# Performance work log

Hardware: AMD Instinct MI355X
Metric: run time of the kernel (lower is better)

## Reference

```python
import jax, jax.numpy as jnp
import numpy as np
import math

B, N, M = 4, 2048, 2048
DIM_Q = DIM_K = DIM_V = 1024
H = 16

def setup_inputs() -> dict:
    key = jax.random.key(0)
    ks = jax.random.split(key, 10)
    s = 0.02
    return {
        "Q": jax.random.normal(ks[0], (B, N, DIM_Q), jnp.float32),
        "K": jax.random.normal(ks[1], (B, M, DIM_K), jnp.float32),
        "Wq": jax.random.normal(ks[2], (DIM_V, DIM_Q), jnp.float32) * s,
        "bq": jax.random.normal(ks[3], (DIM_V,), jnp.float32) * s,
        "Wk": jax.random.normal(ks[4], (DIM_V, DIM_K), jnp.float32) * s,
        "bk": jax.random.normal(ks[5], (DIM_V,), jnp.float32) * s,
        "Wv": jax.random.normal(ks[6], (DIM_V, DIM_K), jnp.float32) * s,
        "bv": jax.random.normal(ks[7], (DIM_V,), jnp.float32) * s,
        "Wo": jax.random.normal(ks[8], (DIM_V, DIM_V), jnp.float32) * s,
        "bo": jax.random.normal(ks[9], (DIM_V,), jnp.float32) * s,
    }

def reference(Q, K, Wq, bq, Wk, bk, Wv, bv, Wo, bo):
    d = DIM_V // H  # head dim
    Qp = Q @ Wq.T + bq            # [B,N,DIM_V]
    Kp = K @ Wk.T + bk            # [B,M,DIM_V]
    Vp = K @ Wv.T + bv            # [B,M,DIM_V]
    # split heads: [B,T,H,d] -> [B,H,T,d]
    Qh = Qp.reshape(B, N, H, d).transpose(0, 2, 1, 3)
    Kh = Kp.reshape(B, M, H, d).transpose(0, 2, 1, 3)
    Vh = Vp.reshape(B, M, H, d).transpose(0, 2, 1, 3)
    # NOTE: original scales by sqrt(dim_V), not sqrt(head_dim)
    scores = jnp.einsum('bhnd,bhmd->bhnm', Qh, Kh) / math.sqrt(DIM_V)
    A = jax.nn.softmax(scores, axis=-1)
    Oh = Qh + jnp.einsum('bhnm,bhmd->bhnd', A, Vh)   # residual with projected Q
    O = Oh.transpose(0, 2, 1, 3).reshape(B, N, DIM_V)
    O = O + jax.nn.relu(O @ Wo.T + bo)
    return O
```

## Files before the change

kernel.cpp:

```cpp
#include <hip/hip_runtime.h>
#include <cstddef>
#include <cstdint>


typedef unsigned short ushort_t;
typedef __attribute__((ext_vector_type(8))) short bf16x8;
typedef __attribute__((ext_vector_type(4))) float floatx4;
typedef __attribute__((ext_vector_type(2))) float f32x2;
typedef __attribute__((ext_vector_type(2))) __bf16 b16x2;
typedef __attribute__((ext_vector_type(4))) unsigned short us4;

__device__ __forceinline__ ushort_t f2bf(float x) {
  union { float f; unsigned u; } v; v.f = x;
  unsigned r = v.u + 0x7FFFu + ((v.u >> 16) & 1u);
  return (ushort_t)(r >> 16);
}
__device__ __forceinline__ float bf2f(ushort_t x) {
  union { unsigned u; float f; } v; v.u = ((unsigned)x) << 16;
  return v.f;
}
__device__ __forceinline__ unsigned pk2(float a, float b) {
  union { float f; unsigned u; } x, y; x.f = a; y.f = b;
  return __builtin_amdgcn_perm(y.u + 0x8000u, x.u + 0x8000u, 0x07060302u);
}
__device__ __forceinline__ unsigned pk2c(float a, float b) {
  union { b16x2 v; unsigned u; } r;
  r.v = __builtin_convertvector((f32x2){a, b}, b16x2);
  return r.u;
}
__device__ __forceinline__ floatx4 mfma16(bf16x8 a, bf16x8 b, floatx4 c) {
  return __builtin_amdgcn_mfma_f32_16x16x32_bf16(a, b, c, 0, 0, 0);
}
__device__ __forceinline__ void gld_lds16(const void* g, void* l) {
  __builtin_amdgcn_global_load_lds(
      (const __attribute__((address_space(1))) unsigned int*)g,
      (__attribute__((address_space(3))) unsigned int*)l, 16, 0, 0);
}

__global__ void cvt6(const float* __restrict__ i0, const float* __restrict__ i1,
                     const float* __restrict__ i2, const float* __restrict__ i3,
                     const float* __restrict__ i4, const float* __restrict__ i5,
                     ushort_t* __restrict__ o0, ushort_t* __restrict__ o1,
                     ushort_t* __restrict__ o2, ushort_t* __restrict__ o3,
                     ushort_t* __restrict__ o4, ushort_t* __restrict__ o5) {
  int z = blockIdx.z;
  const float* in = z == 0 ? i0 : z == 1 ? i1 : z == 2 ? i2 : z == 3 ? i3 : z == 4 ? i4 : i5;
  ushort_t* out = z == 0 ? o0 : z == 1 ? o1 : z == 2 ? o2 : z == 3 ? o3 : z == 4 ? o4 : o5;
  int n8 = (z < 2) ? 1048576 : 131072;
  int i = blockIdx.x * 256 + threadIdx.x;
  if (i < n8) {
    const float4* p = (const float4*)in + (size_t)i * 2;
    float4 a = p[0], b = p[1];
    uint4 o;
    o.x = pk2(a.x, a.y); o.y = pk2(a.z, a.w);
    o.z = pk2(b.x, b.y); o.w = pk2(b.z, b.w);
    *((uint4*)out + i) = o;
  }
}

__global__ __launch_bounds__(256, 2)
void gemm_qkv(const ushort_t* __restrict__ Qb, const ushort_t* __restrict__ Kb,
              const ushort_t* __restrict__ Wqb, const ushort_t* __restrict__ Wkb,
              const ushort_t* __restrict__ Wvb,
              const float* __restrict__ bq, const float* __restrict__ bk,
              const float* __restrict__ bv,
              ushort_t* __restrict__ Qp, ushort_t* __restrict__ Kp,
              ushort_t* __restrict__ Vt)
{
  const int Kd = 1024, Nn = 1024;
  const int z = blockIdx.z;
  const ushort_t* Ab = (z == 0) ? Qb : Kb;
  const ushort_t* Bw = (z == 0) ? Wqb : (z == 1) ? Wkb : Wvb;
  const float* bias  = (z == 0) ? bq : (z == 1) ? bk : bv;

  __shared__ __align__(16) ushort_t As[128][64];
  __shared__ __align__(16) ushort_t Bs[128][64];
  const int tid = threadIdx.x;
  const int lane = tid & 63, wave = tid >> 6;
  const int wm = (wave >> 1) * 64, wn = (wave & 1) * 64;
  const int rq = lane & 15, kg = lane >> 4;

  const int wg = blockIdx.x, xcd = wg & 7, slot = wg >> 3;
  const int by = xcd * 8 + (slot >> 3);
  const int bx = slot & 7;
  const int row0 = by * 128, col0 = bx * 128;

  const int st_sub = lane >> 3;
  const int st_cs  = (lane & 7) ^ st_sub;

  floatx4 acc[4][4];
#pragma unroll
  for (int i = 0; i < 4; ++i)
#pragma unroll
    for (int j = 0; j < 4; ++j) acc[i][j] = (floatx4){0.f, 0.f, 0.f, 0.f};

  for (int k0 = 0; k0 < Kd; k0 += 64) {
    __syncthreads();
#pragma unroll
    for (int r = 0; r < 4; ++r) {
      int i = wave * 4 + r;
      int row = i * 8 + st_sub;
      gld_lds16(Ab + (size_t)(row0 + row) * Kd + k0 + st_cs * 8, (ushort_t*)As + i * 512);
      gld_lds16(Bw + (size_t)(col0 + row) * Kd + k0 + st_cs * 8, (ushort_t*)Bs + i * 512);
    }
    __syncthreads();
#pragma unroll
    for (int kq = 0; kq < 2; ++kq) {
      bf16x8 af[4], bfr[4];
#pragma unroll
      for (int mi = 0; mi < 4; ++mi)
        af[mi] = *(const bf16x8*)&As[wm + mi*16 + rq][((kq*4 + kg) ^ (rq & 7)) * 8];
#pragma unroll
      for (int ni = 0; ni < 4; ++ni)
        bfr[ni] = *(const bf16x8*)&Bs[wn + ni*16 + rq][((kq*4 + kg) ^ (rq & 7)) * 8];
#pragma unroll
      for (int mi = 0; mi < 4; ++mi)
#pragma unroll
        for (int ni = 0; ni < 4; ++ni)
          acc[mi][ni] = mfma16(af[mi], bfr[ni], acc[mi][ni]);
    }
  }

  float bv4[4];
#pragma unroll
  for (int ni = 0; ni < 4; ++ni) bv4[ni] = bias[col0 + wn + ni*16 + rq];

  if (z < 2) {
    ushort_t* Cb = (z == 0) ? Qp : Kp;
#pragma unroll
    for (int mi = 0; mi < 4; ++mi)
#pragma unroll
      for (int ni = 0; ni < 4; ++ni)
#pragma unroll
        for (int rr = 0; rr < 4; ++rr) {
          int row = row0 + wm + mi*16 + kg*4 + rr;
          int col = col0 + wn + ni*16 + rq;
          Cb[(size_t)row * Nn + col] = f2bf(acc[mi][ni][rr] + bv4[ni]);
        }
  } else {
#pragma unroll
    for (int mi = 0; mi < 4; ++mi)
#pragma unroll
      for (int ni = 0; ni < 4; ++ni) {
        int col = col0 + wn + ni*16 + rq;
        int h = col >> 6, dvb = (col >> 4) & 3;
        int kvg = row0 + wm + (mi >> 1) * 32;
        int bI = kvg >> 11, kv = kvg & 2047;
        int t = kv >> 7, c = (kv >> 5) & 3;
        size_t addr = (size_t)(bI * 16 + h) * 131072 + t * 8192
                    + (c * 4 + dvb) * 512 + (kg * 16 + rq) * 8 + (mi & 1) * 4;
        us4 o = { f2bf(acc[mi][ni][0] + bv4[ni]), f2bf(acc[mi][ni][1] + bv4[ni]),
                  f2bf(acc[mi][ni][2] + bv4[ni]), f2bf(acc[mi][ni][3] + bv4[ni]) };
        *(us4*)(Vt + addr) = o;
      }
  }
}

__global__ __launch_bounds__(256, 2)
void gemm_out(const ushort_t* __restrict__ Ob, const ushort_t* __restrict__ Bw,
              const float* __restrict__ bias, float* __restrict__ Out)
{
  const int Kd = 1024, Nn = 1024;
  __shared__ __align__(16) ushort_t As[128][64];
  __shared__ __align__(16) ushort_t Bs[128][64];
  const int tid = threadIdx.x;
  const int lane = tid & 63, wave = tid >> 6;
  const int wm = (wave >> 1) * 64, wn = (wave & 1) * 64;
  const int rq = lane & 15, kg = lane >> 4;

  const int wg = blockIdx.x, xcd = wg & 7, slot = wg >> 3;
  const int by = xcd * 8 + (slot >> 3);
  const int bx = slot & 7;
  const int row0 = by * 128, col0 = bx * 128;

  const int st_sub = lane >> 3;
  const int st_cs  = (lane & 7) ^ st_sub;

  floatx4 acc[4][4];
#pragma unroll
  for (int i = 0; i < 4; ++i)
#pragma unroll
    for (int j = 0; j < 4; ++j) acc[i][j] = (floatx4){0.f, 0.f, 0.f, 0.f};

  for (int k0 = 0; k0 < Kd; k0 += 64) {
    __syncthreads();
#pragma unroll
    for (int r = 0; r < 4; ++r) {
      int i = wave * 4 + r;
      int row = i * 8 + st_sub;
      gld_lds16(Ob + (size_t)(row0 + row) * Kd + k0 + st_cs * 8, (ushort_t*)As + i * 512);
      gld_lds16(Bw + (size_t)(col0 + row) * Kd + k0 + st_cs * 8, (ushort_t*)Bs + i * 512);
    }
    __syncthreads();
#pragma unroll
    for (int kq = 0; kq < 2; ++kq) {
      bf16x8 af[4], bfr[4];
#pragma unroll
      for (int mi = 0; mi < 4; ++mi)
        af[mi] = *(const bf16x8*)&As[wm + mi*16 + rq][((kq*4 + kg) ^ (rq & 7)) * 8];
#pragma unroll
      for (int ni = 0; ni < 4; ++ni)
        bfr[ni] = *(const bf16x8*)&Bs[wn + ni*16 + rq][((kq*4 + kg) ^ (rq & 7)) * 8];
#pragma unroll
      for (int mi = 0; mi < 4; ++mi)
#pragma unroll
        for (int ni = 0; ni < 4; ++ni)
          acc[mi][ni] = mfma16(af[mi], bfr[ni], acc[mi][ni]);
    }
  }

  float bv4[4];
#pragma unroll
  for (int ni = 0; ni < 4; ++ni) bv4[ni] = bias[col0 + wn + ni*16 + rq];
#pragma unroll
  for (int mi = 0; mi < 4; ++mi)
#pragma unroll
    for (int ni = 0; ni < 4; ++ni)
#pragma unroll
      for (int rr = 0; rr < 4; ++rr) {
        int row = row0 + wm + mi*16 + kg*4 + rr;
        int col = col0 + wn + ni*16 + rq;
        size_t idx = (size_t)row * Nn + col;
        float pre = acc[mi][ni][rr] + bv4[ni];
        Out[idx] = bf2f(Ob[idx]) + (pre > 0.f ? pre : 0.f);
      }
}

__global__ __launch_bounds__(256, 2)
void attn_kernel(const ushort_t* __restrict__ Qp,
                 const ushort_t* __restrict__ Kp,
                 const ushort_t* __restrict__ Vt,
                 ushort_t* __restrict__ Ob)
{
  const float sc2 = 0.045084439f;
  const int wg = blockIdx.x, xcd = wg & 7, slot = wg >> 3;
  const int bh = xcd * 8 + (slot >> 4);
  const int qt = slot & 15;
  const int b = bh >> 4, h = bh & 15;
  const int q0 = qt * 128;

  __shared__ __align__(16) ushort_t Ks[2][8192];

  const int tid = threadIdx.x, lane = tid & 63, wq = tid >> 6;
  const int rq = lane & 15, kg = lane >> 4;

  const size_t qkbase = (size_t)(b * 2048) * 1024 + h * 64;
  const ushort_t* vbase = Vt + (size_t)bh * 131072 + lane * 8;

  const int sg_sub = lane >> 3;
  const int sg_csk = (lane & 7) ^ sg_sub;

#pragma unroll
  for (int r = 0; r < 4; ++r) {
    int i = wq * 4 + r;
    int row = i * 8 + sg_sub;
    gld_lds16(Qp + qkbase + (size_t)(q0 + row) * 1024 + sg_csk * 8, &Ks[1][i * 512]);
  }
  __syncthreads();

  auto stage = [&](int kt, int bufi) {
    const int kv0 = kt * 128;
#pragma unroll
    for (int r = 0; r < 4; ++r) {
      int i = wq * 4 + r;
      int rowk = i * 8 + sg_sub;
      gld_lds16(Kp + qkbase + (size_t)(kv0 + rowk) * 1024 + sg_csk * 8,
                &Ks[bufi][i * 512]);
    }
  };
  stage(0, 0);

  bf16x8 aq[2][2];
#pragma unroll
  for (int ni = 0; ni < 2; ++ni)
#pragma unroll
    for (int kq = 0; kq < 2; ++kq) {
      int row = wq * 32 + ni * 16 + rq;
      int ch = (kq * 4 + kg) ^ (rq & 7);
      bf16x8 t = *(const bf16x8*)&Ks[1][row * 64 + ch * 8];
#pragma unroll
      for (int e = 0; e < 8; ++e)
        t[e] = (short)f2bf(bf2f((ushort_t)t[e]) * sc2);
      aq[ni][kq] = t;
    }

  bf16x8 ones;
#pragma unroll
  for (int e = 0; e < 8; ++e) ones[e] = (short)0x3F80;

  const floatx4 zf = (floatx4){0.f, 0.f, 0.f, 0.f};

  floatx4 oacc[2][4];
  floatx4 lacc[2];
#pragma unroll
  for (int nb = 0; nb < 2; ++nb) {
    lacc[nb] = (floatx4){0.f,0.f,0.f,0.f};
#pragma unroll
    for (int dvb = 0; dvb < 4; ++dvb) oacc[nb][dvb] = (floatx4){0.f,0.f,0.f,0.f};
  }

  __syncthreads();

  int cur = 0;
#pragma unroll 2
  for (int kt = 0; kt < 16; ++kt) {
    const ushort_t* vtile = vbase + kt * 8192;

    bf16x8 vfa[16];
#pragma unroll
    for (int j = 0; j < 16; ++j)
      vfa[j] = *(const bf16x8*)(vtile + j * 512);

    if (kt < 15) stage(kt + 1, cur ^ 1);

    floatx4 s[8][2];
    __builtin_amdgcn_s_setprio(1);
    {
      bf16x8 ak[8];
#pragma unroll
      for (int mi = 0; mi < 8; ++mi)
        ak[mi] = *(const bf16x8*)&Ks[cur][(mi * 16 + rq) * 64 + ((kg ^ (rq & 7)) * 8)];
#pragma unroll
      for (int mi = 0; mi < 8; ++mi)
#pragma unroll
        for (int ni = 0; ni < 2; ++ni)
          s[mi][ni] = mfma16(ak[mi], aq[ni][0], zf);
#pragma unroll
      for (int mi = 0; mi < 8; ++mi)
        ak[mi] = *(const bf16x8*)&Ks[cur][(mi * 16 + rq) * 64 + (((4 + kg) ^ (rq & 7)) * 8)];
#pragma unroll
      for (int mi = 0; mi < 8; ++mi)
#pragma unroll
        for (int ni = 0; ni < 2; ++ni)
          s[mi][ni] = mfma16(ak[mi], aq[ni][1], s[mi][ni]);
    }
    __builtin_amdgcn_s_setprio(0);

#pragma unroll
    for (int mi = 0; mi < 2; ++mi)
#pragma unroll
      for (int ni = 0; ni < 2; ++ni)
#pragma unroll
        for (int rr = 0; rr < 4; ++rr)
          s[mi][ni][rr] = __builtin_amdgcn_exp2f(s[mi][ni][rr]);

#pragma unroll
    for (int c = 0; c < 4; ++c) {
      union { unsigned u[4]; bf16x8 v; } pa0, pa1;
      pa0.u[0] = pk2c(s[2*c  ][0][0], s[2*c  ][0][1]);
      pa0.u[1] = pk2c(s[2*c  ][0][2], s[2*c  ][0][3]);
      pa0.u[2] = pk2c(s[2*c+1][0][0], s[2*c+1][0][1]);
      pa0.u[3] = pk2c(s[2*c+1][0][2], s[2*c+1][0][3]);
      pa1.u[0] = pk2c(s[2*c  ][1][0], s[2*c  ][1][1]);
      pa1.u[1] = pk2c(s[2*c  ][1][2], s[2*c  ][1][3]);
      pa1.u[2] = pk2c(s[2*c+1][1][0], s[2*c+1][1][1]);
      pa1.u[3] = pk2c(s[2*c+1][1][2], s[2*c+1][1][3]);
      __builtin_amdgcn_s_setprio(1);
#pragma unroll
      for (int dvb = 0; dvb < 4; ++dvb) {
        oacc[0][dvb] = mfma16(pa0.v, vfa[c*4+dvb], oacc[0][dvb]);
        oacc[1][dvb] = mfma16(pa1.v, vfa[c*4+dvb], oacc[1][dvb]);
      }
      lacc[0] = mfma16(pa0.v, ones, lacc[0]);
      lacc[1] = mfma16(pa1.v, ones, lacc[1]);
      __builtin_amdgcn_s_setprio(0);
      if (c < 3) {
#pragma unroll
        for (int mi = 2*c + 2; mi < 2*c + 4; ++mi)
#pragma unroll
          for (int ni = 0; ni < 2; ++ni)
#pragma unroll
            for (int rr = 0; rr < 4; ++rr)
              s[mi][ni][rr] = __builtin_amdgcn_exp2f(s[mi][ni][rr]);
      }
    }

    __syncthreads();
    cur ^= 1;
  }

#pragma unroll
  for (int nb = 0; nb < 2; ++nb)
#pragma unroll
    for (int rr = 0; rr < 4; ++rr) {
      int row = wq * 32 + nb * 16 + kg * 4 + rr;
      float linv = 1.0f / lacc[nb][rr];
#pragma unroll
      for (int dvb = 0; dvb < 4; ++dvb) {
        int col = dvb * 16 + rq;
        size_t idx = qkbase + (size_t)(q0 + row) * 1024 + col;
        Ob[idx] = f2bf(oacc[nb][dvb][rr] * linv + bf2f(Qp[idx]));
      }
    }
}

extern "C" void kernel_launch(void* const* d_in, const int* in_sizes, int n_in,
                              void* d_out, int out_size, void* d_ws, size_t ws_size,
                              hipStream_t stream)
{
  const float* Q  = (const float*)d_in[0];
  const float* K  = (const float*)d_in[1];
  const float* Wq = (const float*)d_in[2];
  const float* bq = (const float*)d_in[3];
  const float* Wk = (const float*)d_in[4];
  const float* bk = (const float*)d_in[5];
  const float* Wv = (const float*)d_in[6];
  const float* bv = (const float*)d_in[7];
  const float* Wo = (const float*)d_in[8];
  const float* bo = (const float*)d_in[9];
  float* Out = (float*)d_out;

  ushort_t* ws = (ushort_t*)d_ws;
  const size_t E = (size_t)8192 * 1024;
  const size_t WSZ = (size_t)1024 * 1024;
  ushort_t* Qb  = ws;
  ushort_t* Kb  = ws + E;
  ushort_t* Qp  = ws + 2*E;
  ushort_t* Kp  = ws + 3*E;
  ushort_t* Vt  = ws + 4*E;
  ushort_t* Wqb = ws + 5*E;
  ushort_t* Wkb = ws + 5*E + WSZ;
  ushort_t* Wvb = ws + 5*E + 2*WSZ;
  ushort_t* Wob = ws + 5*E + 3*WSZ;
  ushort_t* Ob  = Qb;

  cvt6<<<dim3(4096, 1, 6), 256, 0, stream>>>(Q, K, Wq, Wk, Wv, Wo,
                                             Qb, Kb, Wqb, Wkb, Wvb, Wob);

  dim3 blk(256);
  gemm_qkv<<<dim3(512, 1, 3), blk, 0, stream>>>(Qb, Kb, Wqb, Wkb, Wvb,
                                                bq, bk, bv, Qp, Kp, Vt);
  attn_kernel<<<dim3(1024), blk, 0, stream>>>(Qp, Kp, Vt, Ob);
  gemm_out<<<dim3(512), blk, 0, stream>>>(Ob, Wob, bo, Out);
}
```

Before: 287.7 us.

## Double-buffer LDS tiles in QKV and output projection GEMMs

Both projection GEMM kernels now use two LDS buffers for A and B. The next K-tile is issued via global-to-LDS loads before the MFMA loop runs on the current tile, and only one barrier is kept per iteration. The aim is to hide global load latency behind matrix math and drop one of the two syncs per k-step. LDS use doubles to 64KB per block, which may limit occupancy at two blocks per CU. Correctness depends on the single barrier also waiting for the async LDS loads to finish (vmcnt), which the code does not show explicitly.

```diff
diff --git a/kernel.cpp b/kernel.cpp
--- a/kernel.cpp
+++ b/kernel.cpp
@@ -73,8 +73,8 @@
   const ushort_t* Bw = (z == 0) ? Wqb : (z == 1) ? Wkb : Wvb;
   const float* bias  = (z == 0) ? bq : (z == 1) ? bk : bv;
 
-  __shared__ __align__(16) ushort_t As[128][64];
-  __shared__ __align__(16) ushort_t Bs[128][64];
+  __shared__ __align__(16) ushort_t As[2][8192];
+  __shared__ __align__(16) ushort_t Bs[2][8192];
   const int tid = threadIdx.x;
   const int lane = tid & 63, wave = tid >> 6;
   const int wm = (wave >> 1) * 64, wn = (wave & 1) * 64;
@@ -88,37 +88,45 @@
   const int st_sub = lane >> 3;
   const int st_cs  = (lane & 7) ^ st_sub;
 
-  floatx4 acc[4][4];
-#pragma unroll
-  for (int i = 0; i < 4; ++i)
-#pragma unroll
-    for (int j = 0; j < 4; ++j) acc[i][j] = (floatx4){0.f, 0.f, 0.f, 0.f};
-
-  for (int k0 = 0; k0 < Kd; k0 += 64) {
-    __syncthreads();
+  auto stageAB = [&](int k0, int bufi) {
 #pragma unroll
     for (int r = 0; r < 4; ++r) {
       int i = wave * 4 + r;
       int row = i * 8 + st_sub;
-      gld_lds16(Ab + (size_t)(row0 + row) * Kd + k0 + st_cs * 8, (ushort_t*)As + i * 512);
-      gld_lds16(Bw + (size_t)(col0 + row) * Kd + k0 + st_cs * 8, (ushort_t*)Bs + i * 512);
-    }
-    __syncthreads();
+      gld_lds16(Ab + (size_t)(row0 + row) * Kd + k0 + st_cs * 8, &As[bufi][i * 512]);
+      gld_lds16(Bw + (size_t)(col0 + row) * Kd + k0 + st_cs * 8, &Bs[bufi][i * 512]);
+    }
+  };
+
+  floatx4 acc[4][4];
+#pragma unroll
+  for (int i = 0; i < 4; ++i)
+#pragma unroll
+    for (int j = 0; j < 4; ++j) acc[i][j] = (floatx4){0.f, 0.f, 0.f, 0.f};
+
+  stageAB(0, 0);
+  __syncthreads();
+
+  int cur = 0;
+  for (int kt = 0; kt < 16; ++kt) {
+    if (kt < 15) stageAB((kt + 1) * 64, cur ^ 1);
 #pragma unroll
     for (int kq = 0; kq < 2; ++kq) {
       bf16x8 af[4], bfr[4];
 #pragma unroll
       for (int mi = 0; mi < 4; ++mi)
-        af[mi] = *(const bf16x8*)&As[wm + mi*16 + rq][((kq*4 + kg) ^ (rq & 7)) * 8];
+        af[mi] = *(const bf16x8*)&As[cur][(wm + mi*16 + rq) * 64 + (((kq*4 + kg) ^ (rq & 7)) * 8)];
 #pragma unroll
       for (int ni = 0; ni < 4; ++ni)
-        bfr[ni] = *(const bf16x8*)&Bs[wn + ni*16 + rq][((kq*4 + kg) ^ (rq & 7)) * 8];
+        bfr[ni] = *(const bf16x8*)&Bs[cur][(wn + ni*16 + rq) * 64 + (((kq*4 + kg) ^ (rq & 7)) * 8)];
 #pragma unroll
       for (int mi = 0; mi < 4; ++mi)
 #pragma unroll
         for (int ni = 0; ni < 4; ++ni)
           acc[mi][ni] = mfma16(af[mi], bfr[ni], acc[mi][ni]);
     }
+    __syncthreads();
+    cur ^= 1;
   }
 
   float bv4[4];
@@ -161,8 +169,8 @@
               const float* __restrict__ bias, float* __restrict__ Out)
 {
   const int Kd = 1024, Nn = 1024;
-  __shared__ __align__(16) ushort_t As[128][64];
-  __shared__ __align__(16) ushort_t Bs[128][64];
+  __shared__ __align__(16) ushort_t As[2][8192];
+  __shared__ __align__(16) ushort_t Bs[2][8192];
   const int tid = threadIdx.x;
   const int lane = tid & 63, wave = tid >> 6;
   const int wm = (wave >> 1) * 64, wn = (wave & 1) * 64;
@@ -176,37 +184,45 @@
   const int st_sub = lane >> 3;
   const int st_cs  = (lane & 7) ^ st_sub;
 
-  floatx4 acc[4][4];
-#pragma unroll
-  for (int i = 0; i < 4; ++i)
-#pragma unroll
-    for (int j = 0; j < 4; ++j) acc[i][j] = (floatx4){0.f, 0.f, 0.f, 0.f};
-
-  for (int k0 = 0; k0 < Kd; k0 += 64) {
-    __syncthreads();
+  auto stageAB = [&](int k0, int bufi) {
 #pragma unroll
     for (int r = 0; r < 4; ++r) {
       int i = wave * 4 + r;
       int row = i * 8 + st_sub;
-      gld_lds16(Ob + (size_t)(row0 + row) * Kd + k0 + st_cs * 8, (ushort_t*)As + i * 512);
-      gld_lds16(Bw + (size_t)(col0 + row) * Kd + k0 + st_cs * 8, (ushort_t*)Bs + i * 512);
-    }
-    __syncthreads();
+      gld_lds16(Ob + (size_t)(row0 + row) * Kd + k0 + st_cs * 8, &As[bufi][i * 512]);
+      gld_lds16(Bw + (size_t)(col0 + row) * Kd + k0 + st_cs * 8, &Bs[bufi][i * 512]);
+    }
+  };
+
+  floatx4 acc[4][4];
+#pragma unroll
+  for (int i = 0; i < 4; ++i)
+#pragma unroll
+    for (int j = 0; j < 4; ++j) acc[i][j] = (floatx4){0.f, 0.f, 0.f, 0.f};
+
+  stageAB(0, 0);
+  __syncthreads();
+
+  int cur = 0;
+  for (int kt = 0; kt < 16; ++kt) {
+    if (kt < 15) stageAB((kt + 1) * 64, cur ^ 1);
 #pragma unroll
     for (int kq = 0; kq < 2; ++kq) {
       bf16x8 af[4], bfr[4];
 #pragma unroll
       for (int mi = 0; mi < 4; ++mi)
-        af[mi] = *(const bf16x8*)&As[wm + mi*16 + rq][((kq*4 + kg) ^ (rq & 7)) * 8];
+        af[mi] = *(const bf16x8*)&As[cur][(wm + mi*16 + rq) * 64 + (((kq*4 + kg) ^ (rq & 7)) * 8)];
 #pragma unroll
       for (int ni = 0; ni < 4; ++ni)
-        bfr[ni] = *(const bf16x8*)&Bs[wn + ni*16 + rq][((kq*4 + kg) ^ (rq & 7)) * 8];
+        bfr[ni] = *(const bf16x8*)&Bs[cur][(wn + ni*16 + rq) * 64 + (((kq*4 + kg) ^ (rq & 7)) * 8)];
 #pragma unroll
       for (int mi = 0; mi < 4; ++mi)
 #pragma unroll
         for (int ni = 0; ni < 4; ++ni)
           acc[mi][ni] = mfma16(af[mi], bfr[ni], acc[mi][ni]);
     }
+    __syncthreads();
+    cur ^= 1;
   }
 
   float bv4[4];
```

Result: faster. 277.5 us (-3.6%).
